# Optimization experiments

Measured on AMD Instinct MI355X. Metric: run time of the kernel, lower is better.

Reference implementation:

```python
import jax, jax.numpy as jnp
import numpy as np


def setup_inputs() -> dict:
    key = jax.random.key(0)
    ks = jax.random.split(key, 12)
    B = 131072
    s = lambda fan_in: 1.0 / np.sqrt(fan_in)
    inp = {
        "x": jax.random.normal(ks[0], (B, 2, 13, 21), dtype=jnp.float32),
        # depthwise 3x3, groups=2, no bias: OIHW with O=2, I=1
        "dw_w": jax.random.uniform(ks[1], (2, 1, 3, 3), jnp.float32, -s(9), s(9)),
        # pointwise 1x1: 2 -> 5
        "pw_w": jax.random.uniform(ks[2], (5, 2, 1, 1), jnp.float32, -s(2), s(2)),
        "pw_b": jax.random.uniform(ks[3], (5,), jnp.float32, -s(2), s(2)),
        # conv 1x1: 5 -> 5
        "conv_w": jax.random.uniform(ks[4], (5, 5, 1, 1), jnp.float32, -s(5), s(5)),
        "conv_b": jax.random.uniform(ks[5], (5,), jnp.float32, -s(5), s(5)),
        # dense 90 -> 16 -> 16 -> 14 (torch Linear layout: [out, in])
        "w1": jax.random.uniform(ks[6], (16, 90), jnp.float32, -s(90), s(90)),
        "b1": jax.random.uniform(ks[7], (16,), jnp.float32, -s(90), s(90)),
        "w2": jax.random.uniform(ks[8], (16, 16), jnp.float32, -s(16), s(16)),
        "b2": jax.random.uniform(ks[9], (16,), jnp.float32, -s(16), s(16)),
        "w3": jax.random.uniform(ks[10], (14, 16), jnp.float32, -s(16), s(16)),
        "b3": jax.random.uniform(ks[11], (14,), jnp.float32, -s(16), s(16)),
    }
    return inp


def _conv(x, w, groups=1):
    return jax.lax.conv_general_dilated(
        x, w, window_strides=(1, 1), padding="VALID",
        dimension_numbers=("NCHW", "OIHW", "NCHW"),
        feature_group_count=groups)


def reference(x, dw_w, pw_w, pw_b, conv_w, conv_b, w1, b1, w2, b2, w3, b3):
    # depthwise-separable conv: depthwise 3x3 (groups=2, no bias) + pointwise 1x1
    h = _conv(x, dw_w, groups=2)                      # [B,2,11,19]
    h = _conv(h, pw_w) + pw_b[None, :, None, None]    # [B,5,11,19]
    h = jnp.tanh(h)
    h = _conv(h, conv_w) + conv_b[None, :, None, None]  # 1x1 conv 5->5
    h = jnp.tanh(h)
    # AvgPool2d(3): kernel=stride=3, no padding -> crop to 9x18, reshape-mean
    h = h[:, :, :9, :18]
    B = h.shape[0]
    h = h.reshape(B, 5, 3, 3, 6, 3).mean(axis=(3, 5))  # [B,5,3,6]
    h = jnp.tanh(h)
    h = h.reshape(B, 90)
    h = jnp.tanh(h @ w1.T + b1)
    h = jnp.tanh(h @ w2.T + b2)
    return h @ w3.T + b3                               # [B,14]
```

## Files before the change

### kernel.cpp

```cpp
#include <hip/hip_runtime.h>

typedef float f4v __attribute__((ext_vector_type(4), aligned(4)));
typedef float f2v __attribute__((ext_vector_type(2), aligned(4)));

__device__ __forceinline__ float fast_tanh(float x) {
  float t = x * 2.8853900817779268f;
  float e = __builtin_amdgcn_exp2f(t);
  float r = __builtin_amdgcn_rcpf(e + 1.0f);
  return 1.0f - 2.0f * r;
}

__global__ __launch_bounds__(256, 4) void smartpixel_kernel(
    const float* __restrict__ x, const float* __restrict__ dww,
    const float* __restrict__ pww, const float* __restrict__ pwb,
    const float* __restrict__ cvw, const float* __restrict__ cvb,
    const float* __restrict__ w1, const float* __restrict__ b1,
    const float* __restrict__ w2, const float* __restrict__ b2,
    const float* __restrict__ w3, const float* __restrict__ b3,
    float* __restrict__ out, int nsamp) {
  const int g = blockIdx.x * 256 + threadIdx.x;
  const int s = g >> 2;
  const int t = g & 3;
  if (s >= nsamp) return;

  const int cb = (0x0D090500u >> (8 * t)) & 0xFF;
  const float* xb = x + (long)s * 546 + cb;
  const bool tOdd = (t & 1) != 0;
  const bool isT1 = (t == 1), isT3 = (t == 3);
  const int hT = t >> 1;

  const float kd0 = dww[0], kd1 = dww[1], kd2 = dww[2], kd3 = dww[3], kd4 = dww[4],
              kd5 = dww[5], kd6 = dww[6], kd7 = dww[7], kd8 = dww[8], kd9 = dww[9],
              kd10 = dww[10], kd11 = dww[11], kd12 = dww[12], kd13 = dww[13],
              kd14 = dww[14], kd15 = dww[15], kd16 = dww[16], kd17 = dww[17];
  const float kp0 = pww[0], kp1 = pww[1], kp2 = pww[2], kp3 = pww[3], kp4 = pww[4],
              kp5 = pww[5], kp6 = pww[6], kp7 = pww[7], kp8 = pww[8], kp9 = pww[9];
  const float kb0 = pwb[0], kb1 = pwb[1], kb2 = pwb[2], kb3 = pwb[3], kb4 = pwb[4];
  const float kc0 = cvw[0], kc1 = cvw[1], kc2 = cvw[2], kc3 = cvw[3], kc4 = cvw[4],
              kc5 = cvw[5], kc6 = cvw[6], kc7 = cvw[7], kc8 = cvw[8], kc9 = cvw[9],
              kc10 = cvw[10], kc11 = cvw[11], kc12 = cvw[12], kc13 = cvw[13],
              kc14 = cvw[14], kc15 = cvw[15], kc16 = cvw[16], kc17 = cvw[17],
              kc18 = cvw[18], kc19 = cvw[19], kc20 = cvw[20], kc21 = cvw[21],
              kc22 = cvw[22], kc23 = cvw[23], kc24 = cvw[24];
  const float kcb0 = cvb[0], kcb1 = cvb[1], kcb2 = cvb[2], kcb3 = cvb[3], kcb4 = cvb[4];

#define DECLSLOT(S)                                                          \
  float XA##S##_0, XA##S##_1, XA##S##_2, XA##S##_3, XA##S##_4, XA##S##_5,    \
      XA##S##_6, XA##S##_7, XB##S##_0, XB##S##_1, XB##S##_2, XB##S##_3,      \
      XB##S##_4, XB##S##_5, XB##S##_6, XB##S##_7;
  DECLSLOT(0) DECLSLOT(1) DECLSLOT(2)

#define LDROW(S, PTR)                                                        \
  do {                                                                       \
    const float* p_ = (PTR);                                                 \
    f4v a0_ = *reinterpret_cast<const f4v*>(p_);                             \
    f4v a1_ = *reinterpret_cast<const f4v*>(p_ + 4);                         \
    f4v c0_ = *reinterpret_cast<const f4v*>(p_ + 273);                       \
    f4v c1_ = *reinterpret_cast<const f4v*>(p_ + 277);                       \
    XA##S##_0 = a0_[0]; XA##S##_1 = a0_[1]; XA##S##_2 = a0_[2];              \
    XA##S##_3 = a0_[3]; XA##S##_4 = a1_[0]; XA##S##_5 = a1_[1];              \
    XA##S##_6 = a1_[2]; XA##S##_7 = a1_[3];                                  \
    XB##S##_0 = c0_[0]; XB##S##_1 = c0_[1]; XB##S##_2 = c0_[2];              \
    XB##S##_3 = c0_[3]; XB##S##_4 = c1_[0]; XB##S##_5 = c1_[1];              \
    XB##S##_6 = c1_[2]; XB##S##_7 = c1_[3];                                  \
  } while (0)

  float P0_0 = 0.f, P0_1 = 0.f, P0_2 = 0.f, P0_3 = 0.f, P0_4 = 0.f;
  float P1_0 = 0.f, P1_1 = 0.f, P1_2 = 0.f, P1_3 = 0.f, P1_4 = 0.f;
  float P2_0 = 0.f, P2_1 = 0.f, P2_2 = 0.f, P2_3 = 0.f, P2_4 = 0.f;
  float P3_0 = 0.f, P3_1 = 0.f, P3_2 = 0.f, P3_3 = 0.f, P3_4 = 0.f;
  float P4_0 = 0.f, P4_1 = 0.f, P4_2 = 0.f, P4_3 = 0.f, P4_4 = 0.f;

  float H0 = 0.f, H1 = 0.f, H2 = 0.f, H3 = 0.f, H4 = 0.f, H5 = 0.f, H6 = 0.f,
        H7 = 0.f, H8 = 0.f, H9 = 0.f, H10 = 0.f, H11 = 0.f, H12 = 0.f,
        H13 = 0.f, H14 = 0.f, H15 = 0.f;

#define POS(SA, SB, SC, J0, J1, J2, PP)                                      \
  do {                                                                       \
    float d0 = XA##SA##_##J0 * kd0 + XA##SA##_##J1 * kd1 + XA##SA##_##J2 * kd2 \
             + XA##SB##_##J0 * kd3 + XA##SB##_##J1 * kd4 + XA##SB##_##J2 * kd5 \
             + XA##SC##_##J0 * kd6 + XA##SC##_##J1 * kd7 + XA##SC##_##J2 * kd8; \
    float d1 = XB##SA##_##J0 * kd9 + XB##SA##_##J1 * kd10 + XB##SA##_##J2 * kd11 \
             + XB##SB##_##J0 * kd12 + XB##SB##_##J1 * kd13 + XB##SB##_##J2 * kd14 \
             + XB##SC##_##J0 * kd15 + XB##SC##_##J1 * kd16 + XB##SC##_##J2 * kd17; \
    float u0 = fast_tanh(kb0 + kp0 * d0 + kp1 * d1);                         \
    float u1 = fast_tanh(kb1 + kp2 * d0 + kp3 * d1);                         \
    float u2 = fast_tanh(kb2 + kp4 * d0 + kp5 * d1);                         \
    float u3 = fast_tanh(kb3 + kp6 * d0 + kp7 * d1);                         \
    float u4 = fast_tanh(kb4 + kp8 * d0 + kp9 * d1);                         \
    P0_##PP += fast_tanh(kcb0 + kc0 * u0 + kc1 * u1 + kc2 * u2 + kc3 * u3 + kc4 * u4);   \
    P1_##PP += fast_tanh(kcb1 + kc5 * u0 + kc6 * u1 + kc7 * u2 + kc8 * u3 + kc9 * u4);   \
    P2_##PP += fast_tanh(kcb2 + kc10 * u0 + kc11 * u1 + kc12 * u2 + kc13 * u3 + kc14 * u4); \
    P3_##PP += fast_tanh(kcb3 + kc15 * u0 + kc16 * u1 + kc17 * u2 + kc18 * u3 + kc19 * u4); \
    P4_##PP += fast_tanh(kcb4 + kc20 * u0 + kc21 * u1 + kc22 * u2 + kc23 * u3 + kc24 * u4); \
  } while (0)

#define ROWBODY(SA, SB, SC)                                                  \
  do {                                                                       \
    if (!isT3) POS(SA, SB, SC, 0, 1, 2, 0);                                  \
    POS(SA, SB, SC, 1, 2, 3, 1);                                             \
    POS(SA, SB, SC, 2, 3, 4, 2);                                             \
    POS(SA, SB, SC, 3, 4, 5, 3);                                             \
    if (!isT1) POS(SA, SB, SC, 4, 5, 6, 4);                                  \
  } while (0)

#define ACCH(O)                                                              \
  {                                                                          \
    f2v wv = *reinterpret_cast<const f2v*>(wb_ + (O) * 90);                  \
    H##O += clo * wv[0] + chi * wv[1];                                       \
  }
#define FCH1(C)                                                              \
  do {                                                                       \
    float sA = P##C##_0 + P##C##_1 + P##C##_2;                               \
    float sMe = P##C##_3 + P##C##_4;                                         \
    float sMo = isT3 ? P##C##_1 : P##C##_0;                                  \
    float myMid = tOdd ? sMo : sMe;                                          \
    float sB = P##C##_2 + P##C##_3 + (isT3 ? P##C##_4 : P##C##_1);           \
    float midFull = myMid + __shfl_xor(myMid, 1, 64);                        \
    float pvA = fast_tanh(sA * (1.0f / 9.0f));                               \
    float sHi = tOdd ? sB : midFull;                                         \
    float chi = fast_tanh(sHi * (1.0f / 9.0f));                              \
    float clo = tOdd ? 0.0f : pvA;                                           \
    const float* wb_ = w1 + (C) * 18 + rr6 + hT * 3 + (tOdd ? 1 : 0);        \
    ACCH(0) ACCH(1) ACCH(2) ACCH(3) ACCH(4) ACCH(5) ACCH(6) ACCH(7)          \
    ACCH(8) ACCH(9) ACCH(10) ACCH(11) ACCH(12) ACCH(13) ACCH(14) ACCH(15)    \
    P##C##_0 = 0.f; P##C##_1 = 0.f; P##C##_2 = 0.f; P##C##_3 = 0.f;          \
    P##C##_4 = 0.f;                                                          \
  } while (0)

  LDROW(0, xb);
  LDROW(1, xb + 21);

#pragma unroll 1
  for (int rg = 0; rg < 3; ++rg) {
    const float* xr = xb + rg * 63;
    const int rr6 = rg * 6;
    LDROW(2, xr + 42);
    ROWBODY(0, 1, 2);
    LDROW(0, xr + 63);
    ROWBODY(1, 2, 0);
    LDROW(1, xr + 84);
    ROWBODY(2, 0, 1);
    FCH1(0); FCH1(1); FCH1(2); FCH1(3); FCH1(4);
  }

#define RED(O)                                                               \
  H##O += __shfl_xor(H##O, 1, 64);                                           \
  H##O += __shfl_xor(H##O, 2, 64);                                           \
  H##O = fast_tanh(H##O + b1[O]);
  RED(0) RED(1) RED(2) RED(3) RED(4) RED(5) RED(6) RED(7)
  RED(8) RED(9) RED(10) RED(11) RED(12) RED(13) RED(14) RED(15)

#define FC2(O)                                                               \
  float q##O = fast_tanh(b2[(O)]                                             \
      + H0 * w2[(O) * 16 + 0] + H1 * w2[(O) * 16 + 1] + H2 * w2[(O) * 16 + 2]\
      + H3 * w2[(O) * 16 + 3] + H4 * w2[(O) * 16 + 4] + H5 * w2[(O) * 16 + 5]\
      + H6 * w2[(O) * 16 + 6] + H7 * w2[(O) * 16 + 7] + H8 * w2[(O) * 16 + 8]\
      + H9 * w2[(O) * 16 + 9] + H10 * w2[(O) * 16 + 10]                      \
      + H11 * w2[(O) * 16 + 11] + H12 * w2[(O) * 16 + 12]                    \
      + H13 * w2[(O) * 16 + 13] + H14 * w2[(O) * 16 + 14]                    \
      + H15 * w2[(O) * 16 + 15]);
  FC2(0) FC2(1) FC2(2) FC2(3) FC2(4) FC2(5) FC2(6) FC2(7)
  FC2(8) FC2(9) FC2(10) FC2(11) FC2(12) FC2(13) FC2(14) FC2(15)

  const int base = 4 * t - (hT & (t & 1));
  const float* w3t = w3 + base * 16;
#define DOT3(OO, ROFF)                                                       \
  float o##OO;                                                               \
  {                                                                          \
    f4v wa = *reinterpret_cast<const f4v*>(w3t + (ROFF) + 0);                \
    f4v wb = *reinterpret_cast<const f4v*>(w3t + (ROFF) + 4);                \
    f4v wc = *reinterpret_cast<const f4v*>(w3t + (ROFF) + 8);                \
    f4v wd = *reinterpret_cast<const f4v*>(w3t + (ROFF) + 12);               \
    o##OO = b3[base + (OO)]                                                  \
        + q0 * wa[0] + q1 * wa[1] + q2 * wa[2] + q3 * wa[3]                  \
        + q4 * wb[0] + q5 * wb[1] + q6 * wb[2] + q7 * wb[3]                  \
        + q8 * wc[0] + q9 * wc[1] + q10 * wc[2] + q11 * wc[3]                \
        + q12 * wd[0] + q13 * wd[1] + q14 * wd[2] + q15 * wd[3];             \
  }
  DOT3(0, 0) DOT3(1, 16) DOT3(2, 32)
  float* po = out + (long)s * 14 + base;
  if (t < 2) {
    DOT3(3, 48)
    f4v v; v[0] = o0; v[1] = o1; v[2] = o2; v[3] = o3;
    *reinterpret_cast<f4v*>(po) = v;
  } else if (t == 2) {
    f2v v; v[0] = o0; v[1] = o1;
    *reinterpret_cast<f2v*>(po) = v;
    po[2] = o2;
  } else {
    po[0] = o0;
    f2v v; v[0] = o1; v[1] = o2;
    *reinterpret_cast<f2v*>(po + 1) = v;
  }
}

extern "C" void kernel_launch(void* const* d_in, const int* in_sizes, int n_in,
                              void* d_out, int out_size, void* d_ws, size_t ws_size,
                              hipStream_t stream) {
  const float* x      = (const float*)d_in[0];
  const float* dw_w   = (const float*)d_in[1];
  const float* pw_w   = (const float*)d_in[2];
  const float* pw_b   = (const float*)d_in[3];
  const float* conv_w = (const float*)d_in[4];
  const float* conv_b = (const float*)d_in[5];
  const float* w1     = (const float*)d_in[6];
  const float* b1     = (const float*)d_in[7];
  const float* w2     = (const float*)d_in[8];
  const float* b2     = (const float*)d_in[9];
  const float* w3     = (const float*)d_in[10];
  const float* b3     = (const float*)d_in[11];
  float* out = (float*)d_out;

  int nsamp = in_sizes[0] / 546;
  long nthreads = 4L * nsamp;
  int blocks = (int)((nthreads + 255) / 256);
  smartpixel_kernel<<<blocks, 256, 0, stream>>>(
      x, dw_w, pw_w, pw_b, conv_w, conv_b, w1, b1, w2, b2, w3, b3, out, nsamp);
}
```

Baseline: 136.5 us.

## Fold tanh scaling into weights and split FC2 across lanes with shuffles

Rewrites the tanh chain as sigmoid-style reciprocal forms. The 2*log2(e) scale, the 1-2r affine step and the 1/9 pooling factor are folded into pre-scaled, readfirstlane-broadcast weights and biases, which removes per-element multiplies and FMAs from the hot convolution loop. FC2 is now split so each of the four lanes per sample computes four outputs instead of all sixteen, and the results are gathered with xor shuffles before FC3. This adds shuffle traffic and per-lane indexed w3 loads, and the algebraic refolding may shift floating-point rounding slightly.

```diff
diff --git a/kernel.cpp b/kernel.cpp
--- a/kernel.cpp
+++ b/kernel.cpp
@@ -3,11 +3,20 @@
 typedef float f4v __attribute__((ext_vector_type(4), aligned(4)));
 typedef float f2v __attribute__((ext_vector_type(2), aligned(4)));
 
-__device__ __forceinline__ float fast_tanh(float x) {
-  float t = x * 2.8853900817779268f;
-  float e = __builtin_amdgcn_exp2f(t);
-  float r = __builtin_amdgcn_rcpf(e + 1.0f);
-  return 1.0f - 2.0f * r;
+#define LVAL 2.8853900817779268f
+#define C1P 2.8853900817779268f
+#define C2P -0.6411977959506504f
+
+__device__ __forceinline__ float rfl(float v) {
+  return __int_as_float(__builtin_amdgcn_readfirstlane(__float_as_int(v)));
+}
+__device__ __forceinline__ float rform(float z) {
+  float e = __builtin_amdgcn_exp2f(z);
+  return __builtin_amdgcn_rcpf(e + 1.0f);
+}
+__device__ __forceinline__ float ptanh(float S) {
+  float r = rform(fmaf(C2P, S, C1P));
+  return fmaf(-2.0f, r, 1.0f);
 }
 
 __global__ __launch_bounds__(256, 4) void smartpixel_kernel(
@@ -33,16 +42,23 @@
               kd5 = dww[5], kd6 = dww[6], kd7 = dww[7], kd8 = dww[8], kd9 = dww[9],
               kd10 = dww[10], kd11 = dww[11], kd12 = dww[12], kd13 = dww[13],
               kd14 = dww[14], kd15 = dww[15], kd16 = dww[16], kd17 = dww[17];
-  const float kp0 = pww[0], kp1 = pww[1], kp2 = pww[2], kp3 = pww[3], kp4 = pww[4],
-              kp5 = pww[5], kp6 = pww[6], kp7 = pww[7], kp8 = pww[8], kp9 = pww[9];
-  const float kb0 = pwb[0], kb1 = pwb[1], kb2 = pwb[2], kb3 = pwb[3], kb4 = pwb[4];
-  const float kc0 = cvw[0], kc1 = cvw[1], kc2 = cvw[2], kc3 = cvw[3], kc4 = cvw[4],
-              kc5 = cvw[5], kc6 = cvw[6], kc7 = cvw[7], kc8 = cvw[8], kc9 = cvw[9],
-              kc10 = cvw[10], kc11 = cvw[11], kc12 = cvw[12], kc13 = cvw[13],
-              kc14 = cvw[14], kc15 = cvw[15], kc16 = cvw[16], kc17 = cvw[17],
-              kc18 = cvw[18], kc19 = cvw[19], kc20 = cvw[20], kc21 = cvw[21],
-              kc22 = cvw[22], kc23 = cvw[23], kc24 = cvw[24];
-  const float kcb0 = cvb[0], kcb1 = cvb[1], kcb2 = cvb[2], kcb3 = cvb[3], kcb4 = cvb[4];
+  const float zp0 = rfl(LVAL * pww[0]), zp1 = rfl(LVAL * pww[1]),
+              zp2 = rfl(LVAL * pww[2]), zp3 = rfl(LVAL * pww[3]),
+              zp4 = rfl(LVAL * pww[4]), zp5 = rfl(LVAL * pww[5]),
+              zp6 = rfl(LVAL * pww[6]), zp7 = rfl(LVAL * pww[7]),
+              zp8 = rfl(LVAL * pww[8]), zp9 = rfl(LVAL * pww[9]);
+  const float zb0 = rfl(LVAL * pwb[0]), zb1 = rfl(LVAL * pwb[1]),
+              zb2 = rfl(LVAL * pwb[2]), zb3 = rfl(LVAL * pwb[3]),
+              zb4 = rfl(LVAL * pwb[4]);
+#define ZC(q, p) rfl(-2.0f * LVAL * cvw[5 * (q) + (p)])
+  const float zc0 = ZC(0, 0), zc1 = ZC(0, 1), zc2 = ZC(0, 2), zc3 = ZC(0, 3), zc4 = ZC(0, 4);
+  const float zc5 = ZC(1, 0), zc6 = ZC(1, 1), zc7 = ZC(1, 2), zc8 = ZC(1, 3), zc9 = ZC(1, 4);
+  const float zc10 = ZC(2, 0), zc11 = ZC(2, 1), zc12 = ZC(2, 2), zc13 = ZC(2, 3), zc14 = ZC(2, 4);
+  const float zc15 = ZC(3, 0), zc16 = ZC(3, 1), zc17 = ZC(3, 2), zc18 = ZC(3, 3), zc19 = ZC(3, 4);
+  const float zc20 = ZC(4, 0), zc21 = ZC(4, 1), zc22 = ZC(4, 2), zc23 = ZC(4, 3), zc24 = ZC(4, 4);
+#define ZCB(q) rfl(LVAL * (cvb[q] + cvw[5 * (q)] + cvw[5 * (q) + 1] + cvw[5 * (q) + 2] + \
+                            cvw[5 * (q) + 3] + cvw[5 * (q) + 4]))
+  const float zcb0 = ZCB(0), zcb1 = ZCB(1), zcb2 = ZCB(2), zcb3 = ZCB(3), zcb4 = ZCB(4);
 
 #define DECLSLOT(S)                                                          \
   float XA##S##_0, XA##S##_1, XA##S##_2, XA##S##_3, XA##S##_4, XA##S##_5,    \
@@ -83,16 +99,16 @@
     float d1 = XB##SA##_##J0 * kd9 + XB##SA##_##J1 * kd10 + XB##SA##_##J2 * kd11 \
              + XB##SB##_##J0 * kd12 + XB##SB##_##J1 * kd13 + XB##SB##_##J2 * kd14 \
              + XB##SC##_##J0 * kd15 + XB##SC##_##J1 * kd16 + XB##SC##_##J2 * kd17; \
-    float u0 = fast_tanh(kb0 + kp0 * d0 + kp1 * d1);                         \
-    float u1 = fast_tanh(kb1 + kp2 * d0 + kp3 * d1);                         \
-    float u2 = fast_tanh(kb2 + kp4 * d0 + kp5 * d1);                         \
-    float u3 = fast_tanh(kb3 + kp6 * d0 + kp7 * d1);                         \
-    float u4 = fast_tanh(kb4 + kp8 * d0 + kp9 * d1);                         \
-    P0_##PP += fast_tanh(kcb0 + kc0 * u0 + kc1 * u1 + kc2 * u2 + kc3 * u3 + kc4 * u4);   \
-    P1_##PP += fast_tanh(kcb1 + kc5 * u0 + kc6 * u1 + kc7 * u2 + kc8 * u3 + kc9 * u4);   \
-    P2_##PP += fast_tanh(kcb2 + kc10 * u0 + kc11 * u1 + kc12 * u2 + kc13 * u3 + kc14 * u4); \
-    P3_##PP += fast_tanh(kcb3 + kc15 * u0 + kc16 * u1 + kc17 * u2 + kc18 * u3 + kc19 * u4); \
-    P4_##PP += fast_tanh(kcb4 + kc20 * u0 + kc21 * u1 + kc22 * u2 + kc23 * u3 + kc24 * u4); \
+    float r0 = rform(zb0 + zp0 * d0 + zp1 * d1);                             \
+    float r1 = rform(zb1 + zp2 * d0 + zp3 * d1);                             \
+    float r2 = rform(zb2 + zp4 * d0 + zp5 * d1);                             \
+    float r3 = rform(zb3 + zp6 * d0 + zp7 * d1);                             \
+    float r4 = rform(zb4 + zp8 * d0 + zp9 * d1);                             \
+    P0_##PP += rform(zcb0 + zc0 * r0 + zc1 * r1 + zc2 * r2 + zc3 * r3 + zc4 * r4);     \
+    P1_##PP += rform(zcb1 + zc5 * r0 + zc6 * r1 + zc7 * r2 + zc8 * r3 + zc9 * r4);     \
+    P2_##PP += rform(zcb2 + zc10 * r0 + zc11 * r1 + zc12 * r2 + zc13 * r3 + zc14 * r4); \
+    P3_##PP += rform(zcb3 + zc15 * r0 + zc16 * r1 + zc17 * r2 + zc18 * r3 + zc19 * r4); \
+    P4_##PP += rform(zcb4 + zc20 * r0 + zc21 * r1 + zc22 * r2 + zc23 * r3 + zc24 * r4); \
   } while (0)
 
 #define ROWBODY(SA, SB, SC)                                                  \
@@ -117,9 +133,9 @@
     float myMid = tOdd ? sMo : sMe;                                          \
     float sB = P##C##_2 + P##C##_3 + (isT3 ? P##C##_4 : P##C##_1);           \
     float midFull = myMid + __shfl_xor(myMid, 1, 64);                        \
-    float pvA = fast_tanh(sA * (1.0f / 9.0f));                               \
+    float pvA = ptanh(sA);                                                   \
     float sHi = tOdd ? sB : midFull;                                         \
-    float chi = fast_tanh(sHi * (1.0f / 9.0f));                              \
+    float chi = ptanh(sHi);                                                  \
     float clo = tOdd ? 0.0f : pvA;                                           \
     const float* wb_ = w1 + (C) * 18 + rr6 + hT * 3 + (tOdd ? 1 : 0);        \
     ACCH(0) ACCH(1) ACCH(2) ACCH(3) ACCH(4) ACCH(5) ACCH(6) ACCH(7)          \
@@ -147,36 +163,53 @@
 #define RED(O)                                                               \
   H##O += __shfl_xor(H##O, 1, 64);                                           \
   H##O += __shfl_xor(H##O, 2, 64);                                           \
-  H##O = fast_tanh(H##O + b1[O]);
+  {                                                                          \
+    float rr_ = rform((H##O + b1[O]) * LVAL);                                \
+    H##O = fmaf(-2.0f, rr_, 1.0f);                                           \
+  }
   RED(0) RED(1) RED(2) RED(3) RED(4) RED(5) RED(6) RED(7)
   RED(8) RED(9) RED(10) RED(11) RED(12) RED(13) RED(14) RED(15)
 
-#define FC2(O)                                                               \
-  float q##O = fast_tanh(b2[(O)]                                             \
-      + H0 * w2[(O) * 16 + 0] + H1 * w2[(O) * 16 + 1] + H2 * w2[(O) * 16 + 2]\
-      + H3 * w2[(O) * 16 + 3] + H4 * w2[(O) * 16 + 4] + H5 * w2[(O) * 16 + 5]\
-      + H6 * w2[(O) * 16 + 6] + H7 * w2[(O) * 16 + 7] + H8 * w2[(O) * 16 + 8]\
-      + H9 * w2[(O) * 16 + 9] + H10 * w2[(O) * 16 + 10]                      \
-      + H11 * w2[(O) * 16 + 11] + H12 * w2[(O) * 16 + 12]                    \
-      + H13 * w2[(O) * 16 + 13] + H14 * w2[(O) * 16 + 14]                    \
-      + H15 * w2[(O) * 16 + 15]);
-  FC2(0) FC2(1) FC2(2) FC2(3) FC2(4) FC2(5) FC2(6) FC2(7)
-  FC2(8) FC2(9) FC2(10) FC2(11) FC2(12) FC2(13) FC2(14) FC2(15)
+  const int myo = 4 * t;
+  float g0, g1, g2, g3;
+#define FC2S(I)                                                              \
+  {                                                                          \
+    const float* wr = w2 + (myo + (I)) * 16;                                 \
+    f4v wa = *reinterpret_cast<const f4v*>(wr);                              \
+    f4v wb = *reinterpret_cast<const f4v*>(wr + 4);                          \
+    f4v wc = *reinterpret_cast<const f4v*>(wr + 8);                          \
+    f4v wd = *reinterpret_cast<const f4v*>(wr + 12);                         \
+    float acc = b2[myo + (I)]                                                \
+        + H0 * wa[0] + H1 * wa[1] + H2 * wa[2] + H3 * wa[3]                  \
+        + H4 * wb[0] + H5 * wb[1] + H6 * wb[2] + H7 * wb[3]                  \
+        + H8 * wc[0] + H9 * wc[1] + H10 * wc[2] + H11 * wc[3]                \
+        + H12 * wd[0] + H13 * wd[1] + H14 * wd[2] + H15 * wd[3];             \
+    float rr_ = rform(acc * LVAL);                                           \
+    g##I = fmaf(-2.0f, rr_, 1.0f);                                           \
+  }
+  FC2S(0) FC2S(1) FC2S(2) FC2S(3)
+
+#define GATH(I)                                                              \
+  float hB_##I = __shfl_xor(g##I, 1, 64);                                    \
+  float hC_##I = __shfl_xor(g##I, 2, 64);                                    \
+  float hD_##I = __shfl_xor(hB_##I, 2, 64);
+  GATH(0) GATH(1) GATH(2) GATH(3)
 
   const int base = 4 * t - (hT & (t & 1));
   const float* w3t = w3 + base * 16;
+  const int offA = 4 * t, offB = 4 * (t ^ 1), offC = 4 * (t ^ 2), offD = 4 * (t ^ 3);
 #define DOT3(OO, ROFF)                                                       \
   float o##OO;                                                               \
   {                                                                          \
-    f4v wa = *reinterpret_cast<const f4v*>(w3t + (ROFF) + 0);                \
-    f4v wb = *reinterpret_cast<const f4v*>(w3t + (ROFF) + 4);                \
-    f4v wc = *reinterpret_cast<const f4v*>(w3t + (ROFF) + 8);                \
-    f4v wd = *reinterpret_cast<const f4v*>(w3t + (ROFF) + 12);               \
+    f4v wa = *reinterpret_cast<const f4v*>(w3t + (ROFF) + offA);             \
+    f4v wb = *reinterpret_cast<const f4v*>(w3t + (ROFF) + offB);             \
+    f4v wc = *reinterpret_cast<const f4v*>(w3t + (ROFF) + offC);             \
+    f4v wd = *reinterpret_cast<const f4v*>(w3t + (ROFF) + offD);             \
     o##OO = b3[base + (OO)]                                                  \
-        + q0 * wa[0] + q1 * wa[1] + q2 * wa[2] + q3 * wa[3]                  \
-        + q4 * wb[0] + q5 * wb[1] + q6 * wb[2] + q7 * wb[3]                  \
-        + q8 * wc[0] + q9 * wc[1] + q10 * wc[2] + q11 * wc[3]                \
-        + q12 * wd[0] + q13 * wd[1] + q14 * wd[2] + q15 * wd[3];             \
+        + g0 * wa[0] + g1 * wa[1] + g2 * wa[2] + g3 * wa[3]                  \
+        + hB_0 * wb[0] + hB_1 * wb[1] + hB_2 * wb[2] + hB_3 * wb[3]          \
+        + hC_0 * wc[0] + hC_1 * wc[1] + hC_2 * wc[2] + hC_3 * wc[3]          \
+        + hD_0 * wd[0] + hD_1 * wd[1] + hD_2 * wd[2] + hD_3 * wd[3];         \
   }
   DOT3(0, 0) DOT3(1, 16) DOT3(2, 32)
   float* po = out + (long)s * 14 + base;
```

Measured after the change: 390.9 us. +186.3%, slower.
